# Kernel tuning notes

Measured on AMD Instinct MI355X. Metric: run time of the kernel, lower is better.

The kernel has to match this reference:

```python
import jax, jax.numpy as jnp
import numpy as np

IN_N, IN_D, OUT_N, OUT_D = 2048, 16, 64, 16
LN_EPS = 1e-5

def setup_inputs() -> dict:
    key = jax.random.key(0)
    k1, k2 = jax.random.split(key)
    w_const = np.sqrt(OUT_N / (IN_D * IN_N)).astype(np.float32)
    return {
        "input": jax.random.normal(k1, (128, IN_N, IN_D), dtype=jnp.float32),
        "w": w_const * jax.random.normal(k2, (IN_N, IN_D, OUT_N, OUT_D), dtype=jnp.float32),
        "ln_gamma": jnp.ones((OUT_D,), dtype=jnp.float32),
        "ln_beta": jnp.zeros((OUT_D,), dtype=jnp.float32),
    }

def _squash(x):
    # squash along last dim: (|x|^2/(1+|x|^2)) * x/|x|
    sq = jnp.sum(x * x, axis=-1, keepdims=True)
    return (sq / (1.0 + sq)) * x / jnp.sqrt(sq)

def reference(input, w, ln_gamma, ln_beta):
    b, n, a = input.shape
    m = w.shape[2]
    # query_key=None path: softmax over zeros -> uniform 1/m routing coeffs
    qk = jnp.full((n, m), 1.0 / m, dtype=input.dtype)
    # bmd = sum_{n,a} qk[n,m] * input[b,n,a] * w[n,a,m,d]
    v = jnp.einsum('nm,bna,namd->bmd', qk, input, w)
    v = _squash(v)
    new_qk = jnp.einsum('bna,namd,bmd->bnm', input, w, v)
    # dropout with p=0 (eval) is identity; LayerNorm over out_d_capsules
    mu = jnp.mean(v, axis=-1, keepdims=True)
    var = jnp.mean((v - mu) ** 2, axis=-1, keepdims=True)
    v = (v - mu) / jnp.sqrt(var + LN_EPS) * ln_gamma + ln_beta
    return (new_qk, v)
```

## Files before the change

### kernel.cpp

```cpp
#include <hip/hip_runtime.h>
#include <cstdint>
#include <cstddef>

typedef short bfrag __attribute__((ext_vector_type(8)));
typedef float facc  __attribute__((ext_vector_type(4)));

namespace {
constexpr int B = 128, N = 2048, A = 16, M = 64, D = 16;
constexpr int NA = N * A;
constexpr int MD = M * D;
constexpr size_t C_ELEMS = (size_t)B * MD;
}

static __device__ __forceinline__ ushort f2bf(float x) {
    uint u = __float_as_uint(x);
    u += 0x7fffu + ((u >> 16) & 1u);
    return (ushort)(u >> 16);
}
static __device__ __forceinline__ bfrag ld_frag16(const ushort* p) {
    union { uint4 q; bfrag v; } u;
    u.q = *(const uint4*)p;
    return u.v;
}
static __device__ __forceinline__ bfrag ld_frag4(const ushort* p) {
    const uint* q = (const uint*)p;
    union { uint a[4]; bfrag v; } u;
    u.a[0] = q[0]; u.a[1] = q[1]; u.a[2] = q[2]; u.a[3] = q[3];
    return u.v;
}

__global__ __launch_bounds__(512, 2) void k1_mfma(const float* __restrict__ in,
                                                  const float* __restrict__ w,
                                                  float* __restrict__ part,
                                                  int nch) {
    const int mdg   = blockIdx.x;
    const int chunk = blockIdx.y;
    const int t     = threadIdx.x;
    const int nap   = NA / nch;
    const int nkt   = nap / 64;
    __shared__ __align__(16) ushort in_t[128 * 72];
    __shared__ __align__(16) ushort w_t[256 * 66];
    const int wv = t >> 6, tl = t & 63;
    const int wb = wv >> 2, wm = wv & 3;
    const int lr = tl & 15, hi = tl >> 4;

    facc acc[4][4];
    #pragma unroll
    for (int i = 0; i < 4; ++i)
        #pragma unroll
        for (int j = 0; j < 4; ++j) acc[i][j] = facc{0.f, 0.f, 0.f, 0.f};

    float4 pin[4], pw[8];
    const int ib  = t >> 4, ik = t & 15;
    const int wk  = t >> 6, wmd = t & 63;

    int na0 = (size_t)chunk * nap;
    #pragma unroll
    for (int q = 0; q < 4; ++q)
        pin[q] = *(const float4*)(in + (size_t)(q * 32 + ib) * NA + na0 + ik * 4);
    #pragma unroll
    for (int q = 0; q < 8; ++q)
        pw[q] = *(const float4*)(w + (size_t)(na0 + q * 8 + wk) * MD + mdg * 256 + wmd * 4);

    for (int kt = 0; kt < nkt; ++kt) {
        __syncthreads();
        #pragma unroll
        for (int q = 0; q < 4; ++q) {
            union { ushort s[4]; uint2 u; } pk;
            pk.s[0] = f2bf(pin[q].x); pk.s[1] = f2bf(pin[q].y);
            pk.s[2] = f2bf(pin[q].z); pk.s[3] = f2bf(pin[q].w);
            *(uint2*)(&in_t[(q * 32 + ib) * 72 + ik * 4]) = pk.u;
        }
        #pragma unroll
        for (int q = 0; q < 8; ++q) {
            const int krow = q * 8 + wk;
            w_t[(wmd * 4 + 0) * 66 + krow] = f2bf(pw[q].x);
            w_t[(wmd * 4 + 1) * 66 + krow] = f2bf(pw[q].y);
            w_t[(wmd * 4 + 2) * 66 + krow] = f2bf(pw[q].z);
            w_t[(wmd * 4 + 3) * 66 + krow] = f2bf(pw[q].w);
        }
        __syncthreads();
        if (kt + 1 < nkt) {
            const int nan = na0 + 64;
            #pragma unroll
            for (int q = 0; q < 4; ++q)
                pin[q] = *(const float4*)(in + (size_t)(q * 32 + ib) * NA + nan + ik * 4);
            #pragma unroll
            for (int q = 0; q < 8; ++q)
                pw[q] = *(const float4*)(w + (size_t)(nan + q * 8 + wk) * MD + mdg * 256 + wmd * 4);
        }
        #pragma unroll
        for (int ks = 0; ks < 2; ++ks) {
            bfrag af[4], bf[4];
            #pragma unroll
            for (int bt = 0; bt < 4; ++bt)
                af[bt] = ld_frag16(&in_t[(wb * 64 + bt * 16 + lr) * 72 + ks * 32 + hi * 8]);
            #pragma unroll
            for (int mt = 0; mt < 4; ++mt)
                bf[mt] = ld_frag4(&w_t[(wm * 64 + mt * 16 + lr) * 66 + ks * 32 + hi * 8]);
            #pragma unroll
            for (int bt = 0; bt < 4; ++bt)
                #pragma unroll
                for (int mt = 0; mt < 4; ++mt)
                    acc[bt][mt] = __builtin_amdgcn_mfma_f32_16x16x32_bf16(
                        af[bt], bf[mt], acc[bt][mt], 0, 0, 0);
        }
        na0 += 64;
    }
    #pragma unroll
    for (int bt = 0; bt < 4; ++bt)
        #pragma unroll
        for (int mt = 0; mt < 4; ++mt) {
            const int b  = wb * 64 + bt * 16 + hi * 4;
            const int md = mdg * 256 + wm * 64 + mt * 16 + lr;
            #pragma unroll
            for (int r = 0; r < 4; ++r)
                part[((size_t)chunk * B + b + r) * MD + md] = acc[bt][mt][r];
        }
}

__global__ __launch_bounds__(256) void k2_squash_ln(const float* __restrict__ part,
                                                    const float* __restrict__ gamma,
                                                    const float* __restrict__ beta,
                                                    float* __restrict__ v_sq,
                                                    float* __restrict__ out_v,
                                                    int nch) {
    const int idx = blockIdx.x * 256 + threadIdx.x;
    const int d   = idx & 15;
    float s = 0.f;
    for (int c = 0; c < nch; ++c) s += part[(size_t)c * C_ELEMS + idx];
    const float v = s * (1.0f / 64.0f);
    float sq = v * v;
    #pragma unroll
    for (int off = 1; off < 16; off <<= 1) sq += __shfl_xor(sq, off, 16);
    const float f  = sqrtf(sq) / (1.0f + sq);
    const float vs = v * f;
    v_sq[idx] = vs;
    float mu = vs;
    #pragma unroll
    for (int off = 1; off < 16; off <<= 1) mu += __shfl_xor(mu, off, 16);
    mu *= (1.0f / 16.0f);
    const float dd = vs - mu;
    float var = dd * dd;
    #pragma unroll
    for (int off = 1; off < 16; off <<= 1) var += __shfl_xor(var, off, 16);
    var *= (1.0f / 16.0f);
    out_v[idx] = dd / sqrtf(var + 1e-5f) * gamma[d] + beta[d];
}

__global__ __launch_bounds__(512, 2) void k3_mfma(const float* __restrict__ in,
                                                  const float* __restrict__ w,
                                                  const float* __restrict__ vsq,
                                                  float* __restrict__ qk) {
    const int m0 = blockIdx.x * 16;
    const int n0 = blockIdx.y * 16;
    const int t  = threadIdx.x;
    const int wv = t >> 6, tl = t & 63;
    const int lr = tl & 15, hi = tl >> 4;
    const int b  = wv * 16 + lr;
    __shared__ __align__(16) ushort w_t[2][4096];
    __shared__ __align__(16) ushort in_t[2][2048];

    float4 vsr[16];
    #pragma unroll
    for (int mi = 0; mi < 16; ++mi)
        vsr[mi] = *(const float4*)(vsq + ((size_t)b * M + m0 + mi) * D + hi * 4);

    float4 pw[2], pin;
    auto ldg = [&](int n) {
        #pragma unroll
        for (int q = 0; q < 2; ++q) {
            const int idx = q * 512 + t;
            const int a = idx >> 6, mloc = (idx >> 2) & 15, d4 = idx & 3;
            pw[q] = *(const float4*)(
                w + (((size_t)n * A + a) * M + m0 + mloc) * D + d4 * 4);
        }
        pin = *(const float4*)(in + (size_t)(t >> 2) * NA + n * A + (t & 3) * 4);
    };
    auto stg = [&](int p) {
        #pragma unroll
        for (int q = 0; q < 2; ++q) {
            const int idx = q * 512 + t;
            const int a = idx >> 6, mloc = (idx >> 2) & 15, d4 = idx & 3;
            const int base = mloc * 256 + (a >> 3) * 128 + (a & 7);
            const int swz  = (mloc & 7) << 3;
            w_t[p][(base + (d4 * 4 + 0) * 8) ^ swz] = f2bf(pw[q].x);
            w_t[p][(base + (d4 * 4 + 1) * 8) ^ swz] = f2bf(pw[q].y);
            w_t[p][(base + (d4 * 4 + 2) * 8) ^ swz] = f2bf(pw[q].z);
            w_t[p][(base + (d4 * 4 + 3) * 8) ^ swz] = f2bf(pw[q].w);
        }
        union { ushort s[4]; uint2 u; } pk;
        pk.s[0] = f2bf(pin.x); pk.s[1] = f2bf(pin.y);
        pk.s[2] = f2bf(pin.z); pk.s[3] = f2bf(pin.w);
        *(uint2*)(&in_t[p][(t >> 2) * 16 + (t & 3) * 4]) = pk.u;
    };

    ldg(n0);
    stg(0);
    __syncthreads();
    for (int i = 0; i < 16; ++i) {
        const int p = i & 1;
        if (i + 1 < 16) ldg(n0 + i + 1);
        uint4 braw = *(const uint4*)&in_t[p][b * 16 + (hi & 1) * 8];
        if (hi >= 2) { braw.x = 0u; braw.y = 0u; braw.z = 0u; braw.w = 0u; }
        union { uint4 q; bfrag v; } bu; bu.q = braw;
        const facc zero = facc{0.f, 0.f, 0.f, 0.f};
        float out4[4];
        #pragma unroll
        for (int mi = 0; mi < 16; ++mi) {
            const int ridx = (mi * 256 + (hi & 1) * 128 + lr * 8) ^ ((mi & 7) << 3);
            uint4 araw = *(const uint4*)&w_t[p][ridx];
            if (hi >= 2) { araw.x = 0u; araw.y = 0u; araw.z = 0u; araw.w = 0u; }
            union { uint4 q; bfrag v; } au; au.q = araw;
            const facc c = __builtin_amdgcn_mfma_f32_16x16x32_bf16(au.v, bu.v, zero, 0, 0, 0);
            float s = c[0] * vsr[mi].x + c[1] * vsr[mi].y
                    + c[2] * vsr[mi].z + c[3] * vsr[mi].w;
            s += __shfl_xor(s, 16);
            s += __shfl_xor(s, 32);
            if ((mi >> 2) == hi) out4[mi & 3] = s;
        }
        const float4 o = {out4[0], out4[1], out4[2], out4[3]};
        *(float4*)(qk + ((size_t)b * N + n0 + i) * M + m0 + hi * 4) = o;
        if (i + 1 < 16) {
            stg(p ^ 1);
            __syncthreads();
        }
    }
}

extern "C" void kernel_launch(void* const* d_in, const int* in_sizes, int n_in,
                              void* d_out, int out_size, void* d_ws, size_t ws_size,
                              hipStream_t stream) {
    const float* in    = (const float*)d_in[0];
    const float* w     = (const float*)d_in[1];
    const float* gamma = (const float*)d_in[2];
    const float* beta  = (const float*)d_in[3];
    float* out_qk = (float*)d_out;
    float* out_v  = out_qk + (size_t)B * N * M;

    int nch = 64;
    if (ws_size < (64 + 1) * C_ELEMS * sizeof(float)) nch = 16;
    if (ws_size < (16 + 1) * C_ELEMS * sizeof(float)) nch = 8;
    float* part = (float*)d_ws;
    float* vsq  = part + (size_t)nch * C_ELEMS;

    k1_mfma<<<dim3(4, nch), 512, 0, stream>>>(in, w, part, nch);
    k2_squash_ln<<<(int)(C_ELEMS / 256), 256, 0, stream>>>(part, gamma, beta, vsq, out_v, nch);
    k3_mfma<<<dim3(4, 128), 512, 0, stream>>>(in, w, vsq, out_qk);
}
```

Before: 146.9 us.

## Process two n per pipeline stage with padded LDS layout and deeper prefetch

Restructures k3_mfma so each stage stages two n-slices of w and input into shared memory, using a padded stride-24 layout with zeroed padding. The padding replaces the XOR swizzle and the per-lane masking of the upper K half, since the padding lanes read zeros. Global loads are issued two stages ahead, which halves barrier count per n and gives more latency hiding. The cost is more LDS (about 36KB versus 24KB), more registers for the prefetch buffers, scalar 2-byte LDS stores with possible bank conflicts, and an extra barrier per phase.

After: 138.3 us. 5.8% less time.

```diff
diff --git a/kernel.cpp b/kernel.cpp
--- a/kernel.cpp
+++ b/kernel.cpp
@@ -158,71 +158,90 @@
     const int wv = t >> 6, tl = t & 63;
     const int lr = tl & 15, hi = tl >> 4;
     const int b  = wv * 16 + lr;
-    __shared__ __align__(16) ushort w_t[2][4096];
-    __shared__ __align__(16) ushort in_t[2][2048];
+    __shared__ __align__(16) ushort wt[2][2][6144];
+    __shared__ __align__(16) ushort it[2][2][3072];
+
+    {
+        const uint4 z = {0u, 0u, 0u, 0u};
+        uint4* z1 = (uint4*)&wt[0][0][0];
+        #pragma unroll
+        for (int j = 0; j < 6; ++j) z1[j * 512 + t] = z;
+        uint4* z2 = (uint4*)&it[0][0][0];
+        #pragma unroll
+        for (int j = 0; j < 3; ++j) z2[j * 512 + t] = z;
+    }
 
     float4 vsr[16];
     #pragma unroll
     for (int mi = 0; mi < 16; ++mi)
         vsr[mi] = *(const float4*)(vsq + ((size_t)b * M + m0 + mi) * D + hi * 4);
 
-    float4 pw[2], pin;
-    auto ldg = [&](int n) {
-        #pragma unroll
-        for (int q = 0; q < 2; ++q) {
-            const int idx = q * 512 + t;
-            const int a = idx >> 6, mloc = (idx >> 2) & 15, d4 = idx & 3;
-            pw[q] = *(const float4*)(
-                w + (((size_t)n * A + a) * M + m0 + mloc) * D + d4 * 4);
-        }
-        pin = *(const float4*)(in + (size_t)(t >> 2) * NA + n * A + (t & 3) * 4);
+    const int sa  = t >> 6, smd = t & 63;
+    const int mloc = smd >> 2, d0 = (smd & 3) * 4;
+    const int sb  = t >> 2, saf = t & 3;
+    float4 pw[2][2], pin[2];
+    const int koff = (hi < 2) ? hi * 8 : 16;
+
+    auto ldg = [&](int ph) {
+        #pragma unroll
+        for (int nn = 0; nn < 2; ++nn) {
+            const int n = n0 + ph * 2 + nn;
+            pw[nn][0] = *(const float4*)(
+                w + (size_t)(n * A + sa) * MD + m0 * D + smd * 4);
+            pw[nn][1] = *(const float4*)(
+                w + (size_t)(n * A + sa + 8) * MD + m0 * D + smd * 4);
+            pin[nn] = *(const float4*)(in + (size_t)sb * NA + n * A + saf * 4);
+        }
     };
     auto stg = [&](int p) {
         #pragma unroll
-        for (int q = 0; q < 2; ++q) {
-            const int idx = q * 512 + t;
-            const int a = idx >> 6, mloc = (idx >> 2) & 15, d4 = idx & 3;
-            const int base = mloc * 256 + (a >> 3) * 128 + (a & 7);
-            const int swz  = (mloc & 7) << 3;
-            w_t[p][(base + (d4 * 4 + 0) * 8) ^ swz] = f2bf(pw[q].x);
-            w_t[p][(base + (d4 * 4 + 1) * 8) ^ swz] = f2bf(pw[q].y);
-            w_t[p][(base + (d4 * 4 + 2) * 8) ^ swz] = f2bf(pw[q].z);
-            w_t[p][(base + (d4 * 4 + 3) * 8) ^ swz] = f2bf(pw[q].w);
-        }
-        union { ushort s[4]; uint2 u; } pk;
-        pk.s[0] = f2bf(pin.x); pk.s[1] = f2bf(pin.y);
-        pk.s[2] = f2bf(pin.z); pk.s[3] = f2bf(pin.w);
-        *(uint2*)(&in_t[p][(t >> 2) * 16 + (t & 3) * 4]) = pk.u;
+        for (int nn = 0; nn < 2; ++nn) {
+            ushort* wb_ = &wt[p][nn][0];
+            #pragma unroll
+            for (int h = 0; h < 2; ++h) {
+                const int a = sa + h * 8;
+                wb_[(mloc * 16 + d0 + 0) * 24 + a] = f2bf(pw[nn][h].x);
+                wb_[(mloc * 16 + d0 + 1) * 24 + a] = f2bf(pw[nn][h].y);
+                wb_[(mloc * 16 + d0 + 2) * 24 + a] = f2bf(pw[nn][h].z);
+                wb_[(mloc * 16 + d0 + 3) * 24 + a] = f2bf(pw[nn][h].w);
+            }
+            union { ushort s[4]; uint2 u; } pk;
+            pk.s[0] = f2bf(pin[nn].x); pk.s[1] = f2bf(pin[nn].y);
+            pk.s[2] = f2bf(pin[nn].z); pk.s[3] = f2bf(pin[nn].w);
+            *(uint2*)(&it[p][nn][sb * 24 + saf * 4]) = pk.u;
+        }
     };
 
-    ldg(n0);
+    ldg(0);
+    __syncthreads();
     stg(0);
+    ldg(1);
     __syncthreads();
-    for (int i = 0; i < 16; ++i) {
-        const int p = i & 1;
-        if (i + 1 < 16) ldg(n0 + i + 1);
-        uint4 braw = *(const uint4*)&in_t[p][b * 16 + (hi & 1) * 8];
-        if (hi >= 2) { braw.x = 0u; braw.y = 0u; braw.z = 0u; braw.w = 0u; }
-        union { uint4 q; bfrag v; } bu; bu.q = braw;
-        const facc zero = facc{0.f, 0.f, 0.f, 0.f};
-        float out4[4];
-        #pragma unroll
-        for (int mi = 0; mi < 16; ++mi) {
-            const int ridx = (mi * 256 + (hi & 1) * 128 + lr * 8) ^ ((mi & 7) << 3);
-            uint4 araw = *(const uint4*)&w_t[p][ridx];
-            if (hi >= 2) { araw.x = 0u; araw.y = 0u; araw.z = 0u; araw.w = 0u; }
-            union { uint4 q; bfrag v; } au; au.q = araw;
-            const facc c = __builtin_amdgcn_mfma_f32_16x16x32_bf16(au.v, bu.v, zero, 0, 0, 0);
-            float s = c[0] * vsr[mi].x + c[1] * vsr[mi].y
-                    + c[2] * vsr[mi].z + c[3] * vsr[mi].w;
-            s += __shfl_xor(s, 16);
-            s += __shfl_xor(s, 32);
-            if ((mi >> 2) == hi) out4[mi & 3] = s;
-        }
-        const float4 o = {out4[0], out4[1], out4[2], out4[3]};
-        *(float4*)(qk + ((size_t)b * N + n0 + i) * M + m0 + hi * 4) = o;
-        if (i + 1 < 16) {
+    for (int ph = 0; ph < 8; ++ph) {
+        const int p = ph & 1;
+        #pragma unroll
+        for (int nn = 0; nn < 2; ++nn) {
+            const int n = n0 + ph * 2 + nn;
+            const bfrag bf = ld_frag16(&it[p][nn][b * 24 + koff]);
+            const facc zero = facc{0.f, 0.f, 0.f, 0.f};
+            float out4[4];
+            #pragma unroll
+            for (int mi = 0; mi < 16; ++mi) {
+                const bfrag af = ld_frag16(&wt[p][nn][(mi * 16 + lr) * 24 + koff]);
+                const facc c = __builtin_amdgcn_mfma_f32_16x16x32_bf16(af, bf, zero, 0, 0, 0);
+                float s = c[0] * vsr[mi].x + c[1] * vsr[mi].y
+                        + c[2] * vsr[mi].z + c[3] * vsr[mi].w;
+                s += __shfl_xor(s, 16);
+                s += __shfl_xor(s, 32);
+                if ((mi >> 2) == hi) out4[mi & 3] = s;
+            }
+            const float4 o = {out4[0], out4[1], out4[2], out4[3]};
+            *(float4*)(qk + ((size_t)b * N + n) * M + m0 + hi * 4) = o;
+        }
+        __syncthreads();
+        if (ph < 7) {
             stg(p ^ 1);
+            if (ph < 6) ldg(ph + 2);
             __syncthreads();
         }
     }
```

## Rewrite qk kernel with 32x32x16 MFMA, 8-wide m tiles and split loaders

Applied to the files above, without the earlier changes.

Replaces the third kernel with a version that uses 32x32x16 bf16 MFMA instead of half-masked 16x16x32 MFMA, so no lanes are wasted on zeroed operands. Each block now covers 8 output capsules over 2 n values per phase, with the work split across warps by batch group and n. Half the threads load weights and half load inputs, writing swizzled single-buffered LDS tiles. The grid doubles and the occupancy hint rises to 4 blocks, aiming at better MFMA utilization and more latency hiding. In exchange it adds an extra barrier per phase and puts more pressure on registers.

Result: slower. 168.8 us (+15.0%).

```diff
diff --git a/kernel.cpp b/kernel.cpp
--- a/kernel.cpp
+++ b/kernel.cpp
@@ -2,8 +2,10 @@
 #include <cstdint>
 #include <cstddef>
 
-typedef short bfrag __attribute__((ext_vector_type(8)));
-typedef float facc  __attribute__((ext_vector_type(4)));
+typedef short bfrag  __attribute__((ext_vector_type(8)));
+typedef float facc   __attribute__((ext_vector_type(4)));
+typedef float f32x16 __attribute__((ext_vector_type(16)));
+typedef float f32x4v __attribute__((ext_vector_type(4)));
 
 namespace {
 constexpr int B = 128, N = 2048, A = 16, M = 64, D = 16;
@@ -148,83 +150,111 @@
     out_v[idx] = dd / sqrtf(var + 1e-5f) * gamma[d] + beta[d];
 }
 
-__global__ __launch_bounds__(512, 2) void k3_mfma(const float* __restrict__ in,
-                                                  const float* __restrict__ w,
-                                                  const float* __restrict__ vsq,
-                                                  float* __restrict__ qk) {
-    const int m0 = blockIdx.x * 16;
+__global__ __launch_bounds__(512, 4) void k3_mfma2(const float* __restrict__ in,
+                                                   const float* __restrict__ w,
+                                                   const float* __restrict__ vsq,
+                                                   float* __restrict__ qk) {
+    const int mg = blockIdx.x;
+    const int m0 = mg * 8;
     const int n0 = blockIdx.y * 16;
     const int t  = threadIdx.x;
-    const int wv = t >> 6, tl = t & 63;
-    const int lr = tl & 15, hi = tl >> 4;
-    const int b  = wv * 16 + lr;
-    __shared__ __align__(16) ushort w_t[2][4096];
-    __shared__ __align__(16) ushort in_t[2][2048];
-
-    float4 vsr[16];
-    #pragma unroll
-    for (int mi = 0; mi < 16; ++mi)
-        vsr[mi] = *(const float4*)(vsq + ((size_t)b * M + m0 + mi) * D + hi * 4);
-
-    float4 pw[2], pin;
-    auto ldg = [&](int n) {
-        #pragma unroll
-        for (int q = 0; q < 2; ++q) {
-            const int idx = q * 512 + t;
-            const int a = idx >> 6, mloc = (idx >> 2) & 15, d4 = idx & 3;
-            pw[q] = *(const float4*)(
-                w + (((size_t)n * A + a) * M + m0 + mloc) * D + d4 * 4);
-        }
-        pin = *(const float4*)(in + (size_t)(t >> 2) * NA + n * A + (t & 3) * 4);
+    const int wv = t >> 6;
+    const int bg = wv & 3, nw = wv >> 2;
+    const int lane = t & 63;
+    const int lc = lane & 31, l5 = lane >> 5;
+    const int b  = bg * 32 + lc;
+    const int swb = (lc >> 2) & 1;
+
+    __shared__ __align__(16) ushort wt[4096];
+    __shared__ __align__(16) ushort it[4096];
+
+    f32x4v vr[8][2];
+    #pragma unroll
+    for (int m = 0; m < 8; ++m) {
+        vr[m][0] = *(const f32x4v*)(vsq + ((size_t)b * M + m0 + m) * D + 4 * l5);
+        vr[m][1] = *(const f32x4v*)(vsq + ((size_t)b * M + m0 + m) * D + 8 + 4 * l5);
+    }
+
+    const bool is_w = t < 256;
+    const int  su   = t & 255;
+    const int s_nn = su >> 7, s_a0 = ((su >> 5) & 3) * 4;
+    const int s_m  = (su >> 2) & 7, s_d4 = su & 3;
+    const int s_b  = su >> 1, s_q = su & 1;
+
+    float4 pr[4];
+    auto ldg = [&](int ph) {
+        const int nb = n0 + ph * 2;
+        if (is_w) {
+            const size_t base =
+                (((size_t)(nb + s_nn) * A + s_a0) * M + m0 + s_m) * D + s_d4 * 4;
+            #pragma unroll
+            for (int j = 0; j < 4; ++j)
+                pr[j] = *(const float4*)(w + base + (size_t)j * MD);
+        } else {
+            const float* p = in + (size_t)s_b * NA + (size_t)(nb + s_q) * A;
+            #pragma unroll
+            for (int j = 0; j < 4; ++j) pr[j] = *(const float4*)(p + j * 4);
+        }
     };
-    auto stg = [&](int p) {
-        #pragma unroll
-        for (int q = 0; q < 2; ++q) {
-            const int idx = q * 512 + t;
-            const int a = idx >> 6, mloc = (idx >> 2) & 15, d4 = idx & 3;
-            const int base = mloc * 256 + (a >> 3) * 128 + (a & 7);
-            const int swz  = (mloc & 7) << 3;
-            w_t[p][(base + (d4 * 4 + 0) * 8) ^ swz] = f2bf(pw[q].x);
-            w_t[p][(base + (d4 * 4 + 1) * 8) ^ swz] = f2bf(pw[q].y);
-            w_t[p][(base + (d4 * 4 + 2) * 8) ^ swz] = f2bf(pw[q].z);
-            w_t[p][(base + (d4 * 4 + 3) * 8) ^ swz] = f2bf(pw[q].w);
-        }
-        union { ushort s[4]; uint2 u; } pk;
-        pk.s[0] = f2bf(pin.x); pk.s[1] = f2bf(pin.y);
-        pk.s[2] = f2bf(pin.z); pk.s[3] = f2bf(pin.w);
-        *(uint2*)(&in_t[p][(t >> 2) * 16 + (t & 3) * 4]) = pk.u;
+    auto stg = [&]() {
+        if (is_w) {
+            const int mp = s_m >> 1, mj = s_m & 1;
+            const int h = s_a0 >> 3, ain = s_a0 & 7;
+            const int phys = h ^ (s_d4 & 1);
+            #pragma unroll
+            for (int k = 0; k < 4; ++k) {
+                const int row = mj * 16 + s_d4 * 4 + k;
+                ushort4 v;
+                v.x = f2bf(pr[0][k]); v.y = f2bf(pr[1][k]);
+                v.z = f2bf(pr[2][k]); v.w = f2bf(pr[3][k]);
+                *(ushort4*)(&wt[(s_nn * 4 + mp) * 512 + row * 16 + phys * 8 + ain]) = v;
+            }
+        } else {
+            union { ushort s[8]; uint4 q; } h0, h1;
+            h0.s[0] = f2bf(pr[0].x); h0.s[1] = f2bf(pr[0].y);
+            h0.s[2] = f2bf(pr[0].z); h0.s[3] = f2bf(pr[0].w);
+            h0.s[4] = f2bf(pr[1].x); h0.s[5] = f2bf(pr[1].y);
+            h0.s[6] = f2bf(pr[1].z); h0.s[7] = f2bf(pr[1].w);
+            h1.s[0] = f2bf(pr[2].x); h1.s[1] = f2bf(pr[2].y);
+            h1.s[2] = f2bf(pr[2].z); h1.s[3] = f2bf(pr[2].w);
+            h1.s[4] = f2bf(pr[3].x); h1.s[5] = f2bf(pr[3].y);
+            h1.s[6] = f2bf(pr[3].z); h1.s[7] = f2bf(pr[3].w);
+            const int sw = (s_b >> 2) & 1;
+            const int base = (s_q * 128 + s_b) * 16;
+            *(uint4*)(&it[base + sw * 8])       = h0.q;
+            *(uint4*)(&it[base + (1 - sw) * 8]) = h1.q;
+        }
     };
 
-    ldg(n0);
-    stg(0);
-    __syncthreads();
-    for (int i = 0; i < 16; ++i) {
-        const int p = i & 1;
-        if (i + 1 < 16) ldg(n0 + i + 1);
-        uint4 braw = *(const uint4*)&in_t[p][b * 16 + (hi & 1) * 8];
-        if (hi >= 2) { braw.x = 0u; braw.y = 0u; braw.z = 0u; braw.w = 0u; }
-        union { uint4 q; bfrag v; } bu; bu.q = braw;
-        const facc zero = facc{0.f, 0.f, 0.f, 0.f};
-        float out4[4];
-        #pragma unroll
-        for (int mi = 0; mi < 16; ++mi) {
-            const int ridx = (mi * 256 + (hi & 1) * 128 + lr * 8) ^ ((mi & 7) << 3);
-            uint4 araw = *(const uint4*)&w_t[p][ridx];
-            if (hi >= 2) { araw.x = 0u; araw.y = 0u; araw.z = 0u; araw.w = 0u; }
-            union { uint4 q; bfrag v; } au; au.q = araw;
-            const facc c = __builtin_amdgcn_mfma_f32_16x16x32_bf16(au.v, bu.v, zero, 0, 0, 0);
-            float s = c[0] * vsr[mi].x + c[1] * vsr[mi].y
-                    + c[2] * vsr[mi].z + c[3] * vsr[mi].w;
-            s += __shfl_xor(s, 16);
-            s += __shfl_xor(s, 32);
-            if ((mi >> 2) == hi) out4[mi & 3] = s;
-        }
-        const float4 o = {out4[0], out4[1], out4[2], out4[3]};
-        *(float4*)(qk + ((size_t)b * N + n0 + i) * M + m0 + hi * 4) = o;
-        if (i + 1 < 16) {
-            stg(p ^ 1);
-            __syncthreads();
-        }
+    ldg(0);
+    for (int ph = 0; ph < 8; ++ph) {
+        __syncthreads();
+        stg();
+        __syncthreads();
+        if (ph < 7) ldg(ph + 1);
+
+        const int n = n0 + ph * 2 + nw;
+        const bfrag bf = ld_frag16(&it[(nw * 128 + b) * 16 + (l5 ^ swb) * 8]);
+        float sreg[8];
+        #pragma unroll
+        for (int mp = 0; mp < 4; ++mp) {
+            const bfrag af = ld_frag16(
+                &wt[(nw * 4 + mp) * 512 + lc * 16 + (l5 ^ swb) * 8]);
+            f32x16 c = {};
+            c = __builtin_amdgcn_mfma_f32_32x32x16_bf16(af, bf, c, 0, 0, 0);
+            #pragma unroll
+            for (int mj = 0; mj < 2; ++mj) {
+                float s = 0.f;
+                #pragma unroll
+                for (int rr = 0; rr < 8; ++rr)
+                    s += c[mj * 8 + rr] * vr[mp * 2 + mj][rr >> 2][rr & 3];
+                s += __shfl_xor(s, 32);
+                sreg[mp * 2 + mj] = s;
+            }
+        }
+        const float4 o = l5 ? float4{sreg[4], sreg[5], sreg[6], sreg[7]}
+                            : float4{sreg[0], sreg[1], sreg[2], sreg[3]};
+        *(float4*)(qk + ((size_t)b * N + n) * M + m0 + l5 * 4) = o;
     }
 }
 
@@ -246,5 +276,5 @@
 
     k1_mfma<<<dim3(4, nch), 512, 0, stream>>>(in, w, part, nch);
     k2_squash_ln<<<(int)(C_ELEMS / 256), 256, 0, stream>>>(part, gamma, beta, vsq, out_v, nch);
-    k3_mfma<<<dim3(4, 128), 512, 0, stream>>>(in, w, vsq, out_qk);
-}
+    k3_mfma2<<<dim3(8, 128), 512, 0, stream>>>(in, w, vsq, out_qk);
+}
```
